# Kernel optimization log

Measured on AMD Instinct MI355X. Metric: run time of the kernel, lower is better.

The kernel has to match this reference:

```python
import jax, jax.numpy as jnp
import numpy as np

N = 8192   # nodes per graph batch
D = 128    # node_feat_dim
E = 131072 # edges per graph batch
B = 64     # graphs per batch


def _linear_init(k, fin, fout):
    s = 1.0 / np.sqrt(fin)
    kw, kb = jax.random.split(k)
    W = jax.random.uniform(kw, (fin, fout), jnp.float32, -s, s)
    b = jax.random.uniform(kb, (fout,), jnp.float32, -s, s)
    return W, b


def setup_inputs() -> dict:
    key = jax.random.key(0)
    ks = jax.random.split(key, 10)
    x1 = jax.random.normal(ks[0], (N, D), jnp.float32)
    x2 = jax.random.normal(ks[1], (N, D), jnp.float32)
    edge_index1 = jax.random.randint(ks[2], (2, E), 0, N)
    edge_index2 = jax.random.randint(ks[3], (2, E), 0, N)
    # block-contiguous graph ids; every graph id present on both sides
    batch = jnp.arange(N, dtype=jnp.int32) // (N // B)
    mW1, mb1 = _linear_init(ks[4], 2 * D, 512)
    mW2, mb2 = _linear_init(ks[5], 512, 256)  # 256 == 2*D (update_net constraint)
    uW1, ub1 = _linear_init(ks[6], 4 * D, 512)
    uW2, ub2 = _linear_init(ks[7], 512, 256)
    uW3, ub3 = _linear_init(ks[8], 256, D)
    return dict(x1=x1, edge_index1=edge_index1, batch1=batch,
                x2=x2, edge_index2=edge_index2, batch2=batch,
                mW1=mW1, mb1=mb1, mW2=mW2, mb2=mb2,
                uW1=uW1, ub1=ub1, uW2=uW2, ub2=ub2, uW3=uW3, ub3=ub3)


def _message_aggr(x, edge_index, mW1, mb1, mW2, mb2):
    tgt, src = edge_index[0], edge_index[1]
    inp = jnp.concatenate([x[src], x[tgt]], axis=-1)          # [E, 2D]
    msg = jax.nn.relu(inp @ mW1 + mb1) @ mW2 + mb2            # [E, 2D]
    return jax.ops.segment_sum(msg, tgt, num_segments=x.shape[0])


def _cross_attention(x1, batch1, x2, batch2):
    scores = x1 @ x2.T                                        # [N1, N2]
    mask = batch1[:, None] == batch2[None, :]
    scores = jnp.where(mask, scores, -jnp.inf)
    att1 = x1 - jax.nn.softmax(scores, axis=1) @ x2
    att2 = x2 - jax.nn.softmax(scores, axis=0).T @ x1
    return att1, att2


def _node_update(x, messages, attentions, uW1, ub1, uW2, ub2, uW3, ub3):
    u = jnp.concatenate([messages, attentions, x], axis=-1)   # [N, 4D]
    h = jax.nn.relu(u @ uW1 + ub1)
    h = jax.nn.relu(h @ uW2 + ub2)
    return x + h @ uW3 + ub3                                  # residual update


def reference(x1, edge_index1, batch1, x2, edge_index2, batch2,
              mW1, mb1, mW2, mb2, uW1, ub1, uW2, ub2, uW3, ub3):
    m1 = _message_aggr(x1, edge_index1, mW1, mb1, mW2, mb2)
    m2 = _message_aggr(x2, edge_index2, mW1, mb1, mW2, mb2)
    a1, a2 = _cross_attention(x1, batch1, x2, batch2)
    new_x1 = _node_update(x1, m1, a1, uW1, ub1, uW2, ub2, uW3, ub3)
    new_x2 = _node_update(x2, m2, a2, uW1, ub1, uW2, ub2, uW3, ub3)
    return new_x1, new_x2
```

## Files before the change

### kernel.cpp

```cpp
#include <hip/hip_runtime.h>
#include <stdint.h>


typedef unsigned short u16;
typedef __bf16 bf16x8 __attribute__((ext_vector_type(8)));
typedef float f32x4 __attribute__((ext_vector_type(4)));

#define NN 8192
#define DD 128
#define EE 131072
#define GS 128
#define NG 64

__device__ __forceinline__ float bf2f(u16 u){
  return __uint_as_float(((uint32_t)u) << 16);
}
__device__ __forceinline__ u16 f2bf(float f){
  uint32_t x = __float_as_uint(f);
  return (u16)((x + 0x7fffu + ((x >> 16) & 1u)) >> 16);
}
__device__ __forceinline__ void gload16(const u16* g, u16* l){
  __builtin_amdgcn_global_load_lds(
      (const __attribute__((address_space(1))) uint32_t*)(uintptr_t)g,
      (__attribute__((address_space(3))) uint32_t*)(uintptr_t)l, 16, 0, 0);
}

template<bool RELU, bool DEGBIAS, bool RES, typename OT>
__device__ __forceinline__ void gemm_body(
    const u16* __restrict__ A, int lda,
    const u16* __restrict__ Wt, const float* __restrict__ bias,
    const int* __restrict__ deg,
    const float* __restrict__ res1, const float* __restrict__ res2,
    OT* __restrict__ out, int ldc, int K, int bx, int by,
    u16* __restrict__ sh, int t)
{
  u16* As0 = sh;         u16* Bs0 = sh + 4096;
  u16* As1 = sh + 8192;  u16* Bs1 = sh + 12288;
  const int brow = by << 7, bcol = bx << 7;
  const int w = t >> 6, lane = t & 63;
  const int rb = (w >> 1) << 6, cb = (w & 1) << 6;
  const int lr = lane & 15, lq = lane >> 4;

  f32x4 acc[4][4];
  #pragma unroll
  for (int i = 0; i < 4; i++)
    #pragma unroll
    for (int j = 0; j < 4; j++) acc[i][j] = (f32x4){0.f, 0.f, 0.f, 0.f};

  const int s0 = t, s1 = t + 256;
  const int sw0 = (((s0 & 3) ^ ((s0 >> 2) & 3)) << 3);
  const int sw1 = (((s1 & 3) ^ ((s1 >> 2) & 3)) << 3);
  const u16* Ag0 = A  + (size_t)(brow + (s0 >> 2)) * lda + sw0;
  const u16* Ag1 = A  + (size_t)(brow + (s1 >> 2)) * lda + sw1;
  const u16* Bg0 = Wt + (size_t)(bcol + (s0 >> 2)) * K   + sw0;
  const u16* Bg1 = Wt + (size_t)(bcol + (s1 >> 2)) * K   + sw1;
  const int d0 = s0 << 3, d1 = s1 << 3;

  auto stage = [&](int kb, u16* Al, u16* Bl){
    gload16(Ag0 + kb, Al + d0);
    gload16(Ag1 + kb, Al + d1);
    gload16(Bg0 + kb, Bl + d0);
    gload16(Bg1 + kb, Bl + d1);
  };
  auto fence = [&](){
    asm volatile("s_waitcnt vmcnt(0)" ::: "memory");
    __builtin_amdgcn_s_barrier();
    __builtin_amdgcn_sched_barrier(0);
  };
  const int swr = ((lq ^ (lr & 3)) << 3);
  auto compute = [&](const u16* Asb, const u16* Bsb){
    bf16x8 af[4], bfr[4];
    #pragma unroll
    for (int mi = 0; mi < 4; mi++)
      af[mi] = *(const bf16x8*)&Asb[(rb + mi * 16 + lr) * 32 + swr];
    #pragma unroll
    for (int ni = 0; ni < 4; ni++)
      bfr[ni] = *(const bf16x8*)&Bsb[(cb + ni * 16 + lr) * 32 + swr];
    #pragma unroll
    for (int mi = 0; mi < 4; mi++)
      #pragma unroll
      for (int ni = 0; ni < 4; ni++)
        acc[mi][ni] = __builtin_amdgcn_mfma_f32_16x16x32_bf16(af[mi], bfr[ni], acc[mi][ni], 0, 0, 0);
  };

  stage(0, As0, Bs0);
  fence();
  for (int kb = 0; kb < K; kb += 64){
    if (kb + 32 < K) stage(kb + 32, As1, Bs1);
    compute(As0, Bs0);
    fence();
    if (kb + 64 < K) stage(kb + 64, As0, Bs0);
    compute(As1, Bs1);
    fence();
  }

  #pragma unroll
  for (int mi = 0; mi < 4; mi++)
    #pragma unroll
    for (int ni = 0; ni < 4; ni++)
      #pragma unroll
      for (int rr = 0; rr < 4; rr++){
        int grow = brow + rb + mi * 16 + lq * 4 + rr;
        int gcol = bcol + cb + ni * 16 + lr;
        float v = acc[mi][ni][rr];
        if (bias) v += DEGBIAS ? (float)deg[grow] * bias[gcol] : bias[gcol];
        if constexpr (RELU) v = fmaxf(v, 0.f);
        if constexpr (RES){
          const float* rp = (grow < NN) ? res1 : res2;
          v += rp[(size_t)(grow & (NN - 1)) * ldc + gcol];
        }
        if constexpr (sizeof(OT) == 2) out[(size_t)grow * ldc + gcol] = (OT)f2bf(v);
        else                           out[(size_t)grow * ldc + gcol] = (OT)v;
      }
}

template<bool RELU, bool RES, typename OT>
__global__ __launch_bounds__(256)
void gemm2_k(const u16* __restrict__ A, int lda,
             const u16* __restrict__ Wt, const float* __restrict__ bias,
             const float* __restrict__ res1, const float* __restrict__ res2,
             OT* __restrict__ out, int ldc, int K)
{
  __shared__ u16 sh[16384];
  gemm_body<RELU,false,RES,OT>(A, lda, Wt, bias, nullptr, res1, res2,
                               out, ldc, K, blockIdx.y, blockIdx.x,
                               sh, threadIdx.x);
}

__global__ __launch_bounds__(256)
void pre_k(const float* __restrict__ mW1, const float* __restrict__ mb1,
           const float* __restrict__ mW2, const float* __restrict__ uW1,
           const float* __restrict__ uW2, const float* __restrict__ uW3,
           const float* __restrict__ x1, const float* __restrict__ x2,
           const int* __restrict__ ei1, const int* __restrict__ ei2,
           u16* __restrict__ WtPQ, float* __restrict__ bPQ,
           u16* __restrict__ Wtm2, u16* __restrict__ Wtu1,
           u16* __restrict__ Wtu2, u16* __restrict__ Wtu3,
           u16* __restrict__ xb, u16* __restrict__ xt,
           u16* __restrict__ U, int* __restrict__ deg)
{
  __shared__ u16 T[8704];
  int b = blockIdx.x, t = threadIdx.x;
  if (b < 2692){
    if (b < 512){
      int idx = b * 256 + t; int c = idx >> 7, k = idx & 127;
      int row = (c < 512) ? k : 128 + k;
      WtPQ[idx] = f2bf(mW1[(size_t)row * 512 + (c & 511)]);
    } else if (b < 1024){
      int idx = (b - 512) * 256 + t; int c = idx >> 9, k = idx & 511;
      Wtm2[idx] = f2bf(mW2[(size_t)k * 256 + c]);
    } else if (b < 2048){
      int idx = (b - 1024) * 256 + t; int c = idx >> 9, k = idx & 511;
      Wtu1[idx] = f2bf(uW1[(size_t)k * 512 + c]);
    } else if (b < 2560){
      int idx = (b - 2048) * 256 + t; int c = idx >> 9, k = idx & 511;
      Wtu2[idx] = f2bf(uW2[(size_t)k * 256 + c]);
    } else if (b < 2688){
      int idx = (b - 2560) * 256 + t; int c = idx >> 8, k = idx & 255;
      Wtu3[idx] = f2bf(uW3[(size_t)k * 128 + c]);
    } else {
      int idx = (b - 2688) * 256 + t;
      bPQ[idx] = (idx < 512) ? 0.f : mb1[idx - 512];
    }
  } else if (b < 4740){
    int a = b - 2692;
    int side = a >> 10, blk = a & 1023;
    const float* x = side ? x2 : x1;
    int i4 = blk * 256 + t;
    float4 v = *(const float4*)&x[(size_t)i4 * 4];
    uint2 pk;
    pk.x = (uint32_t)f2bf(v.x) | ((uint32_t)f2bf(v.y) << 16);
    pk.y = (uint32_t)f2bf(v.z) | ((uint32_t)f2bf(v.w) << 16);
    *(uint2*)&xb[(size_t)side * NN * DD + (size_t)i4 * 4] = pk;
    int n = i4 >> 5, d = (i4 << 2) & 127;
    *(uint2*)&U[((size_t)side * NN + n) * 512 + 384 + d] = pk;
  } else if (b < 4996){
    int a = b - 4740;
    int side = a >> 7, blk = a & 127;
    const float* x = side ? x2 : x1;
    u16* dst = xt + (size_t)side * DD * NN;
    const int n0 = blk * 64;
    #pragma unroll
    for (int i = 0; i < 8; i++){
      int s = i * 256 + t;
      int r = s >> 5, c4 = (s & 31) << 2;
      float4 v = *(const float4*)&x[(size_t)(n0 + r) * DD + c4];
      uint2 pk;
      pk.x = (uint32_t)f2bf(v.x) | ((uint32_t)f2bf(v.y) << 16);
      pk.y = (uint32_t)f2bf(v.z) | ((uint32_t)f2bf(v.w) << 16);
      *(uint2*)&T[r * 136 + c4] = pk;
    }
    __syncthreads();
    #pragma unroll
    for (int i = 0; i < 8; i++){
      int s = i * 256 + t;
      int d = s >> 4, n4 = (s & 15) << 2;
      uint32_t a0 = T[(n4 + 0) * 136 + d];
      uint32_t a1 = T[(n4 + 1) * 136 + d];
      uint32_t a2 = T[(n4 + 2) * 136 + d];
      uint32_t a3 = T[(n4 + 3) * 136 + d];
      uint2 pk; pk.x = a0 | (a1 << 16); pk.y = a2 | (a3 << 16);
      *(uint2*)(dst + (size_t)d * NN + n0 + n4) = pk;
    }
  } else {
    int a = b - 4996;
    int side = a >> 9, blk = a & 511;
    const int* ei = side ? ei2 : ei1;
    int e = blk * 256 + t;
    atomicAdd(&deg[side * NN + ei[e]], 1);
  }
}

__global__ __launch_bounds__(256)
void scan_k(const int* __restrict__ deg,
            int* __restrict__ offs1, int* __restrict__ cur1,
            int* __restrict__ offs2, int* __restrict__ cur2){
  const int* d = deg + blockIdx.x * NN;
  int* offs = blockIdx.x ? offs2 : offs1;
  int* cur  = blockIdx.x ? cur2  : cur1;
  __shared__ int part[256];
  const int t = threadIdx.x;
  const int base = t * 32;
  int loc[32];
  int s = 0;
  #pragma unroll
  for (int i = 0; i < 32; i++){ loc[i] = s; s += d[base + i]; }
  part[t] = s;
  __syncthreads();
  for (int off = 1; off < 256; off <<= 1){
    int v = (t >= off) ? part[t - off] : 0;
    __syncthreads();
    part[t] += v;
    __syncthreads();
  }
  int pre = (t == 0) ? 0 : part[t - 1];
  #pragma unroll
  for (int i = 0; i < 32; i++){
    int o = pre + loc[i];
    offs[base + i] = o;
    cur[base + i]  = o;
  }
  if (t == 255) offs[NN] = part[255];
}

__global__ __launch_bounds__(256)
void mid_k(const u16* __restrict__ xb, const u16* __restrict__ WtPQ,
           const float* __restrict__ bPQ, u16* __restrict__ PQ,
           const int* __restrict__ ei1, const int* __restrict__ ei2,
           int* __restrict__ cur1, int* __restrict__ cur2,
           int* __restrict__ srt1, int* __restrict__ srt2)
{
  __shared__ u16 sh[16384];
  const int b = blockIdx.x, t = threadIdx.x;
  if (b < 1024){
    gemm_body<false,false,false,u16>(xb, 128, WtPQ, bPQ, nullptr, nullptr, nullptr,
                                     PQ, 1024, 128, b >> 7, b & 127, sh, t);
  } else {
    int a = b - 1024;
    int side = a >> 9, blk = a & 511;
    const int* ei = side ? ei2 : ei1;
    int* cur = side ? cur2 : cur1;
    int* srt = side ? srt2 : srt1;
    int e = blk * 256 + t;
    int tgt = ei[e], src = ei[EE + e];
    int p = atomicAdd(&cur[tgt], 1);
    srt[p] = src;
  }
}

__global__ __launch_bounds__(256)
void gather_k(const int* __restrict__ offs1, const int* __restrict__ srt1,
              const int* __restrict__ offs2, const int* __restrict__ srt2,
              const u16* __restrict__ PQ, u16* __restrict__ S)
{
  const int side = blockIdx.y;
  const int* offs = side ? offs2 : offs1;
  const int* srt  = side ? srt2  : srt1;
  const u16* base = PQ + (size_t)side * NN * 1024;
  u16* Sb = S + (size_t)side * NN * 512;

  const int node = (blockIdx.x << 2) + (threadIdx.x >> 6);
  const int lane = threadIdx.x & 63;
  const int beg = offs[node], end = offs[node + 1];

  uint4 qv = *(const uint4*)(base + (size_t)node * 1024 + 512 + (lane << 3));
  float q[8];
  {
    uint32_t qw[4] = {qv.x, qv.y, qv.z, qv.w};
    #pragma unroll
    for (int i = 0; i < 4; i++){
      q[i * 2]     = bf2f((u16)(qw[i] & 0xffffu));
      q[i * 2 + 1] = bf2f((u16)(qw[i] >> 16));
    }
  }
  float acc[8] = {0.f,0.f,0.f,0.f,0.f,0.f,0.f,0.f};

  int e = beg;
  for (; e + 3 < end; e += 4){
    int sA = srt[e], sB = srt[e+1], sC = srt[e+2], sD = srt[e+3];
    uint4 pA = *(const uint4*)(base + (size_t)sA * 1024 + (lane << 3));
    uint4 pB = *(const uint4*)(base + (size_t)sB * 1024 + (lane << 3));
    uint4 pC = *(const uint4*)(base + (size_t)sC * 1024 + (lane << 3));
    uint4 pD = *(const uint4*)(base + (size_t)sD * 1024 + (lane << 3));
    uint32_t aw[4] = {pA.x, pA.y, pA.z, pA.w};
    uint32_t bw[4] = {pB.x, pB.y, pB.z, pB.w};
    uint32_t cw[4] = {pC.x, pC.y, pC.z, pC.w};
    uint32_t dw[4] = {pD.x, pD.y, pD.z, pD.w};
    #pragma unroll
    for (int i = 0; i < 4; i++){
      acc[i*2]   += fmaxf(bf2f((u16)(aw[i] & 0xffffu)) + q[i*2],   0.f)
                  + fmaxf(bf2f((u16)(bw[i] & 0xffffu)) + q[i*2],   0.f)
                  + fmaxf(bf2f((u16)(cw[i] & 0xffffu)) + q[i*2],   0.f)
                  + fmaxf(bf2f((u16)(dw[i] & 0xffffu)) + q[i*2],   0.f);
      acc[i*2+1] += fmaxf(bf2f((u16)(aw[i] >> 16))     + q[i*2+1], 0.f)
                  + fmaxf(bf2f((u16)(bw[i] >> 16))     + q[i*2+1], 0.f)
                  + fmaxf(bf2f((u16)(cw[i] >> 16))     + q[i*2+1], 0.f)
                  + fmaxf(bf2f((u16)(dw[i] >> 16))     + q[i*2+1], 0.f);
    }
  }
  for (; e < end; e++){
    int sA = srt[e];
    uint4 pA = *(const uint4*)(base + (size_t)sA * 1024 + (lane << 3));
    uint32_t aw[4] = {pA.x, pA.y, pA.z, pA.w};
    #pragma unroll
    for (int i = 0; i < 4; i++){
      acc[i*2]   += fmaxf(bf2f((u16)(aw[i] & 0xffffu)) + q[i*2],   0.f);
      acc[i*2+1] += fmaxf(bf2f((u16)(aw[i] >> 16))     + q[i*2+1], 0.f);
    }
  }
  uint4 pk;
  pk.x = (uint32_t)f2bf(acc[0]) | ((uint32_t)f2bf(acc[1]) << 16);
  pk.y = (uint32_t)f2bf(acc[2]) | ((uint32_t)f2bf(acc[3]) << 16);
  pk.z = (uint32_t)f2bf(acc[4]) | ((uint32_t)f2bf(acc[5]) << 16);
  pk.w = (uint32_t)f2bf(acc[6]) | ((uint32_t)f2bf(acc[7]) << 16);
  *(uint4*)(Sb + (size_t)node * 512 + (lane << 3)) = pk;
}

__global__ __launch_bounds__(256)
void msgattn_k(const u16* __restrict__ S, const u16* __restrict__ Wtm2,
               const float* __restrict__ mb2, const int* __restrict__ deg,
               const u16* __restrict__ xb, const u16* __restrict__ xt,
               u16* __restrict__ U)
{
  __shared__ u16 sh[26112];
  const int b = blockIdx.x, t = threadIdx.x;
  if (b < 256){
    gemm_body<false,true,false,u16>(S, 512, Wtm2, mb2, deg, nullptr, nullptr,
                                    U, 512, 512, b >> 7, b & 127, sh, t);
    return;
  }
  const int a = b - 256;
  const int side = a >> 7;
  const int g = a & 63, h = (a >> 6) & 1;
  const u16* Xa = xb + (size_t)side * NN * DD;
  const u16* Xb = xb + (size_t)(1 - side) * NN * DD;
  const u16* Xt = xt + (size_t)(1 - side) * DD * NN;
  u16* Uside = U + (size_t)side * NN * 512;

  u16* XaS = sh;
  u16* XbS = sh + 8704;

  const int w = t >> 6, lane = t & 63;
  const int lr = lane & 15, lq = lane >> 4;

  {
    const u16* sa = Xa + ((size_t)g * GS + h * 64) * DD;
    #pragma unroll
    for (int i = 0; i < 4; i++){
      int s = i * 256 + t; int r = s >> 4, c8 = (s & 15) << 3;
      *(uint4*)&XaS[r * 136 + c8] = *(const uint4*)(sa + (size_t)r * DD + c8);
    }
    const u16* sb = Xb + (size_t)g * GS * DD;
    #pragma unroll
    for (int i = 0; i < 8; i++){
      int s = i * 256 + t; int r = s >> 4, c8 = (s & 15) << 3;
      *(uint4*)&XbS[r * 136 + c8] = *(const uint4*)(sb + (size_t)r * DD + c8);
    }
  }
  __syncthreads();

  f32x4 sc[8];
  #pragma unroll
  for (int ct = 0; ct < 8; ct++) sc[ct] = (f32x4){0.f, 0.f, 0.f, 0.f};
  #pragma unroll
  for (int kb = 0; kb < 4; kb++){
    bf16x8 aa = *(const bf16x8*)&XaS[(w * 16 + lr) * 136 + kb * 32 + (lq << 3)];
    #pragma unroll
    for (int ct = 0; ct < 8; ct++){
      bf16x8 bb = *(const bf16x8*)&XbS[(ct * 16 + lr) * 136 + kb * 32 + (lq << 3)];
      sc[ct] = __builtin_amdgcn_mfma_f32_16x16x32_bf16(aa, bb, sc[ct], 0, 0, 0);
    }
  }
  float inv[4];
  #pragma unroll
  for (int rr = 0; rr < 4; rr++){
    float m = sc[0][rr];
    #pragma unroll
    for (int ct = 1; ct < 8; ct++) m = fmaxf(m, sc[ct][rr]);
    #pragma unroll
    for (int sh_ = 1; sh_ < 16; sh_ <<= 1) m = fmaxf(m, __shfl_xor(m, sh_, 64));
    float s = 0.f;
    #pragma unroll
    for (int ct = 0; ct < 8; ct++){
      float e = __expf(sc[ct][rr] - m);
      sc[ct][rr] = e; s += e;
    }
    #pragma unroll
    for (int sh_ = 1; sh_ < 16; sh_ <<= 1) s += __shfl_xor(s, sh_, 64);
    inv[rr] = 1.f / s;
  }
  #pragma unroll
  for (int ct = 0; ct < 8; ct++)
    #pragma unroll
    for (int rr = 0; rr < 4; rr++)
      XaS[(w * 16 + lq * 4 + rr) * 136 + ct * 16 + lr] = f2bf(sc[ct][rr] * inv[rr]);
  __syncthreads();

  f32x4 o[8];
  #pragma unroll
  for (int ct = 0; ct < 8; ct++) o[ct] = (f32x4){0.f, 0.f, 0.f, 0.f};
  #pragma unroll
  for (int kb = 0; kb < 4; kb++){
    bf16x8 aa = *(const bf16x8*)&XaS[(w * 16 + lr) * 136 + kb * 32 + (lq << 3)];
    #pragma unroll
    for (int ct = 0; ct < 8; ct++){
      bf16x8 bb = *(const bf16x8*)(Xt + (size_t)(ct * 16 + lr) * NN + g * GS + kb * 32 + (lq << 3));
      o[ct] = __builtin_amdgcn_mfma_f32_16x16x32_bf16(aa, bb, o[ct], 0, 0, 0);
    }
  }
  const u16* XaG = Xa + ((size_t)g * GS + h * 64) * DD;
  #pragma unroll
  for (int ct = 0; ct < 8; ct++)
    #pragma unroll
    for (int rr = 0; rr < 4; rr++){
      int row = w * 16 + lq * 4 + rr, col = ct * 16 + lr;
      float xa = bf2f(XaG[(size_t)row * DD + col]);
      Uside[((size_t)g * GS + h * 64 + row) * 512 + 256 + col] = f2bf(xa - o[ct][rr]);
    }
}

extern "C" void kernel_launch(void* const* d_in, const int* in_sizes, int n_in,
                              void* d_out, int out_size, void* d_ws, size_t ws_size,
                              hipStream_t stream)
{
  const float* x1  = (const float*)d_in[0];
  const int*   ei1 = (const int*)  d_in[1];
  const float* x2  = (const float*)d_in[3];
  const int*   ei2 = (const int*)  d_in[4];
  const float* mW1 = (const float*)d_in[6];
  const float* mb1 = (const float*)d_in[7];
  const float* mW2 = (const float*)d_in[8];
  const float* mb2 = (const float*)d_in[9];
  const float* uW1 = (const float*)d_in[10];
  const float* ub1 = (const float*)d_in[11];
  const float* uW2 = (const float*)d_in[12];
  const float* ub2 = (const float*)d_in[13];
  const float* uW3 = (const float*)d_in[14];
  const float* ub3 = (const float*)d_in[15];
  float* out = (float*)d_out;

  char* w = (char*)d_ws;
  auto alloc = [&](size_t b){ char* p = w; w += (b + 255) & ~(size_t)255; return p; };
  u16*  S    = (u16*)alloc((size_t)2 * NN * 512 * 2);
  u16*  PQ   = (u16*)alloc((size_t)2 * NN * 1024 * 2);
  u16*  xb   = (u16*)alloc((size_t)2 * NN * DD * 2);
  u16*  xt   = (u16*)alloc((size_t)2 * DD * NN * 2);
  u16*  U    = (u16*)alloc((size_t)2 * NN * 512 * 2);
  u16*  H1   = (u16*)alloc((size_t)2 * NN * 512 * 2);
  u16*  H2   = (u16*)alloc((size_t)2 * NN * 256 * 2);
  int*  deg  = (int*)alloc((size_t)2 * NN * 4);
  int*  offs1 = (int*)alloc((NN + 1) * 4);
  int*  offs2 = (int*)alloc((NN + 1) * 4);
  int*  cur1  = (int*)alloc(NN * 4);
  int*  cur2  = (int*)alloc(NN * 4);
  int*  srt1  = (int*)alloc((size_t)EE * 4);
  int*  srt2  = (int*)alloc((size_t)EE * 4);
  u16*  WtPQ = (u16*)alloc(1024 * 128 * 2);
  float* bPQ = (float*)alloc(1024 * 4);
  u16*  Wtm2 = (u16*)alloc(256 * 512 * 2);
  u16*  Wtu1 = (u16*)alloc(512 * 512 * 2);
  u16*  Wtu2 = (u16*)alloc(256 * 512 * 2);
  u16*  Wtu3 = (u16*)alloc(128 * 256 * 2);

  hipMemsetAsync(deg, 0, (size_t)2 * NN * 4, stream);

  pre_k<<<4996 + 1024, 256, 0, stream>>>(
      mW1, mb1, mW2, uW1, uW2, uW3, x1, x2, ei1, ei2,
      WtPQ, bPQ, Wtm2, Wtu1, Wtu2, Wtu3, xb, xt, U, deg);

  scan_k<<<2, 256, 0, stream>>>(deg, offs1, cur1, offs2, cur2);

  mid_k<<<2048, 256, 0, stream>>>(xb, WtPQ, bPQ, PQ, ei1, ei2,
                                  cur1, cur2, srt1, srt2);

  gather_k<<<dim3(NN / 4, 2), 256, 0, stream>>>(offs1, srt1, offs2, srt2, PQ, S);

  msgattn_k<<<512, 256, 0, stream>>>(S, Wtm2, mb2, deg, xb, xt, U);

  gemm2_k<true,false,u16><<<dim3(128,4),256,0,stream>>>(
      U, 512, Wtu1, ub1, nullptr, nullptr, H1, 512, 512);
  gemm2_k<true,false,u16><<<dim3(128,2),256,0,stream>>>(
      H1, 512, Wtu2, ub2, nullptr, nullptr, H2, 256, 512);
  gemm2_k<false,true,float><<<dim3(128,1),256,0,stream>>>(
      H2, 256, Wtu3, ub3, x1, x2, out, 128, 256);
}
```

Before: 271.2 us.

## Fuse three node-update GEMMs into one kernel with LDS-resident intermediates

Replaces the three separate update-MLP GEMM launches with a single kernel. Each 512-thread block takes 64 rows and keeps the H1 and H2 activations in shared memory instead of writing them to and reading them back from global memory. The gather loop also gains an 8-edge unrolled path so more independent loads are in flight. The catch is a large LDS footprint (about 138 KB) and only 256 blocks, which lowers occupancy, and each block re-streams the full weight matrices.

```diff
diff --git a/kernel.cpp b/kernel.cpp
--- a/kernel.cpp
+++ b/kernel.cpp
@@ -23,6 +23,11 @@
   __builtin_amdgcn_global_load_lds(
       (const __attribute__((address_space(1))) uint32_t*)(uintptr_t)g,
       (__attribute__((address_space(3))) uint32_t*)(uintptr_t)l, 16, 0, 0);
+}
+__device__ __forceinline__ void gfence(){
+  asm volatile("s_waitcnt vmcnt(0)" ::: "memory");
+  __builtin_amdgcn_s_barrier();
+  __builtin_amdgcn_sched_barrier(0);
 }
 
 template<bool RELU, bool DEGBIAS, bool RES, typename OT>
@@ -62,11 +67,6 @@
     gload16(Bg0 + kb, Bl + d0);
     gload16(Bg1 + kb, Bl + d1);
   };
-  auto fence = [&](){
-    asm volatile("s_waitcnt vmcnt(0)" ::: "memory");
-    __builtin_amdgcn_s_barrier();
-    __builtin_amdgcn_sched_barrier(0);
-  };
   const int swr = ((lq ^ (lr & 3)) << 3);
   auto compute = [&](const u16* Asb, const u16* Bsb){
     bf16x8 af[4], bfr[4];
@@ -84,14 +84,14 @@
   };
 
   stage(0, As0, Bs0);
-  fence();
+  gfence();
   for (int kb = 0; kb < K; kb += 64){
     if (kb + 32 < K) stage(kb + 32, As1, Bs1);
     compute(As0, Bs0);
-    fence();
+    gfence();
     if (kb + 64 < K) stage(kb + 64, As0, Bs0);
     compute(As1, Bs1);
-    fence();
+    gfence();
   }
 
   #pragma unroll
@@ -112,19 +112,6 @@
         if constexpr (sizeof(OT) == 2) out[(size_t)grow * ldc + gcol] = (OT)f2bf(v);
         else                           out[(size_t)grow * ldc + gcol] = (OT)v;
       }
-}
-
-template<bool RELU, bool RES, typename OT>
-__global__ __launch_bounds__(256)
-void gemm2_k(const u16* __restrict__ A, int lda,
-             const u16* __restrict__ Wt, const float* __restrict__ bias,
-             const float* __restrict__ res1, const float* __restrict__ res2,
-             OT* __restrict__ out, int ldc, int K)
-{
-  __shared__ u16 sh[16384];
-  gemm_body<RELU,false,RES,OT>(A, lda, Wt, bias, nullptr, res1, res2,
-                               out, ldc, K, blockIdx.y, blockIdx.x,
-                               sh, threadIdx.x);
 }
 
 __global__ __launch_bounds__(256)
@@ -296,26 +283,40 @@
   float acc[8] = {0.f,0.f,0.f,0.f,0.f,0.f,0.f,0.f};
 
   int e = beg;
+  for (; e + 7 < end; e += 8){
+    int sx[8];
+    #pragma unroll
+    for (int i = 0; i < 8; i++) sx[i] = srt[e + i];
+    uint4 pv[8];
+    #pragma unroll
+    for (int i = 0; i < 8; i++)
+      pv[i] = *(const uint4*)(base + (size_t)sx[i] * 1024 + (lane << 3));
+    #pragma unroll
+    for (int i = 0; i < 8; i++){
+      uint32_t w0[4] = {pv[i].x, pv[i].y, pv[i].z, pv[i].w};
+      #pragma unroll
+      for (int j = 0; j < 4; j++){
+        acc[j*2]   += fmaxf(bf2f((u16)(w0[j] & 0xffffu)) + q[j*2],   0.f);
+        acc[j*2+1] += fmaxf(bf2f((u16)(w0[j] >> 16))     + q[j*2+1], 0.f);
+      }
+    }
+  }
   for (; e + 3 < end; e += 4){
-    int sA = srt[e], sB = srt[e+1], sC = srt[e+2], sD = srt[e+3];
-    uint4 pA = *(const uint4*)(base + (size_t)sA * 1024 + (lane << 3));
-    uint4 pB = *(const uint4*)(base + (size_t)sB * 1024 + (lane << 3));
-    uint4 pC = *(const uint4*)(base + (size_t)sC * 1024 + (lane << 3));
-    uint4 pD = *(const uint4*)(base + (size_t)sD * 1024 + (lane << 3));
-    uint32_t aw[4] = {pA.x, pA.y, pA.z, pA.w};
-    uint32_t bw[4] = {pB.x, pB.y, pB.z, pB.w};
-    uint32_t cw[4] = {pC.x, pC.y, pC.z, pC.w};
-    uint32_t dw[4] = {pD.x, pD.y, pD.z, pD.w};
+    int sx[4];
+    #pragma unroll
+    for (int i = 0; i < 4; i++) sx[i] = srt[e + i];
+    uint4 pv[4];
+    #pragma unroll
+    for (int i = 0; i < 4; i++)
+      pv[i] = *(const uint4*)(base + (size_t)sx[i] * 1024 + (lane << 3));
     #pragma unroll
     for (int i = 0; i < 4; i++){
-      acc[i*2]   += fmaxf(bf2f((u16)(aw[i] & 0xffffu)) + q[i*2],   0.f)
-                  + fmaxf(bf2f((u16)(bw[i] & 0xffffu)) + q[i*2],   0.f)
-                  + fmaxf(bf2f((u16)(cw[i] & 0xffffu)) + q[i*2],   0.f)
-                  + fmaxf(bf2f((u16)(dw[i] & 0xffffu)) + q[i*2],   0.f);
-      acc[i*2+1] += fmaxf(bf2f((u16)(aw[i] >> 16))     + q[i*2+1], 0.f)
-                  + fmaxf(bf2f((u16)(bw[i] >> 16))     + q[i*2+1], 0.f)
-                  + fmaxf(bf2f((u16)(cw[i] >> 16))     + q[i*2+1], 0.f)
-                  + fmaxf(bf2f((u16)(dw[i] >> 16))     + q[i*2+1], 0.f);
+      uint32_t w0[4] = {pv[i].x, pv[i].y, pv[i].z, pv[i].w};
+      #pragma unroll
+      for (int j = 0; j < 4; j++){
+        acc[j*2]   += fmaxf(bf2f((u16)(w0[j] & 0xffffu)) + q[j*2],   0.f);
+        acc[j*2+1] += fmaxf(bf2f((u16)(w0[j] >> 16))     + q[j*2+1], 0.f);
+      }
     }
   }
   for (; e < end; e++){
@@ -437,6 +438,181 @@
       float xa = bf2f(XaG[(size_t)row * DD + col]);
       Uside[((size_t)g * GS + h * 64 + row) * 512 + 256 + col] = f2bf(xa - o[ct][rr]);
     }
+}
+
+__global__ __launch_bounds__(512)
+void upd_k(const u16* __restrict__ U,
+           const u16* __restrict__ Wtu1, const float* __restrict__ ub1,
+           const u16* __restrict__ Wtu2, const float* __restrict__ ub2,
+           const u16* __restrict__ Wtu3, const float* __restrict__ ub3,
+           const float* __restrict__ x1, const float* __restrict__ x2,
+           float* __restrict__ out)
+{
+  __shared__ u16 sh[70656];
+  u16* H1s  = sh;
+  u16* H2s  = sh + 33280;
+  u16* Bst0 = sh + 50176;
+  u16* Bst1 = sh + 58368;
+  u16* Ast0 = sh + 66560;
+  u16* Ast1 = sh + 68608;
+
+  const int t = threadIdx.x;
+  const int w = t >> 6, lane = t & 63;
+  const int wr = w >> 2, wc = w & 3;
+  const int lr = lane & 15, lq = lane >> 4;
+  const int r0 = blockIdx.x << 6;
+
+  const int sA = t;
+  const int rA = sA >> 2;
+  const int swA = (((sA & 3) ^ (rA & 3)) << 3);
+  const int sB0 = t, sB1 = t + 512;
+  const int cB0 = sB0 >> 2, cB1 = sB1 >> 2;
+  const int swB0 = (((sB0 & 3) ^ (cB0 & 3)) << 3);
+  const int swB1 = (((sB1 & 3) ^ (cB1 & 3)) << 3);
+  const int swr = ((lq ^ (lr & 3)) << 3);
+
+  f32x4 acc[2][4];
+  auto zacc = [&](){
+    #pragma unroll
+    for (int i = 0; i < 2; i++)
+      #pragma unroll
+      for (int j = 0; j < 4; j++) acc[i][j] = (f32x4){0.f, 0.f, 0.f, 0.f};
+  };
+
+  for (int hN = 0; hN < 2; hN++){
+    zacc();
+    auto stA = [&](int kb, u16* dst){
+      if (t < 256) gload16(U + (size_t)(r0 + rA) * 512 + kb + swA, dst + sA * 8);
+    };
+    auto stB = [&](int kb, u16* dst){
+      gload16(Wtu1 + (size_t)(hN * 256 + cB0) * 512 + kb + swB0, dst + sB0 * 8);
+      gload16(Wtu1 + (size_t)(hN * 256 + cB1) * 512 + kb + swB1, dst + sB1 * 8);
+    };
+    auto comp = [&](const u16* Asb, const u16* Bsb){
+      bf16x8 af[2], bfv[4];
+      #pragma unroll
+      for (int mi = 0; mi < 2; mi++)
+        af[mi] = *(const bf16x8*)&Asb[(wr * 32 + mi * 16 + lr) * 32 + swr];
+      #pragma unroll
+      for (int ct = 0; ct < 4; ct++)
+        bfv[ct] = *(const bf16x8*)&Bsb[(wc * 64 + ct * 16 + lr) * 32 + swr];
+      #pragma unroll
+      for (int mi = 0; mi < 2; mi++)
+        #pragma unroll
+        for (int ct = 0; ct < 4; ct++)
+          acc[mi][ct] = __builtin_amdgcn_mfma_f32_16x16x32_bf16(af[mi], bfv[ct], acc[mi][ct], 0, 0, 0);
+    };
+    stA(0, Ast0); stB(0, Bst0);
+    gfence();
+    for (int kb = 0; kb < 512; kb += 64){
+      if (kb + 32 < 512){ stA(kb + 32, Ast1); stB(kb + 32, Bst1); }
+      comp(Ast0, Bst0);
+      gfence();
+      if (kb + 64 < 512){ stA(kb + 64, Ast0); stB(kb + 64, Bst0); }
+      comp(Ast1, Bst1);
+      gfence();
+    }
+    #pragma unroll
+    for (int mi = 0; mi < 2; mi++)
+      #pragma unroll
+      for (int ct = 0; ct < 4; ct++)
+        #pragma unroll
+        for (int rr = 0; rr < 4; rr++){
+          int row = wr * 32 + mi * 16 + lq * 4 + rr;
+          int col = wc * 64 + ct * 16 + lr;
+          float v = acc[mi][ct][rr] + ub1[hN * 256 + col];
+          H1s[row * 520 + hN * 256 + col] = f2bf(fmaxf(v, 0.f));
+        }
+  }
+  __syncthreads();
+
+  zacc();
+  {
+    auto stB = [&](int kb, u16* dst){
+      gload16(Wtu2 + (size_t)cB0 * 512 + kb + swB0, dst + sB0 * 8);
+      gload16(Wtu2 + (size_t)cB1 * 512 + kb + swB1, dst + sB1 * 8);
+    };
+    auto comp = [&](int kb, const u16* Bsb){
+      bf16x8 af[2], bfv[4];
+      #pragma unroll
+      for (int mi = 0; mi < 2; mi++)
+        af[mi] = *(const bf16x8*)&H1s[(wr * 32 + mi * 16 + lr) * 520 + kb + (lq << 3)];
+      #pragma unroll
+      for (int ct = 0; ct < 4; ct++)
+        bfv[ct] = *(const bf16x8*)&Bsb[(wc * 64 + ct * 16 + lr) * 32 + swr];
+      #pragma unroll
+      for (int mi = 0; mi < 2; mi++)
+        #pragma unroll
+        for (int ct = 0; ct < 4; ct++)
+          acc[mi][ct] = __builtin_amdgcn_mfma_f32_16x16x32_bf16(af[mi], bfv[ct], acc[mi][ct], 0, 0, 0);
+    };
+    stB(0, Bst0);
+    gfence();
+    for (int kb = 0; kb < 512; kb += 64){
+      if (kb + 32 < 512) stB(kb + 32, Bst1);
+      comp(kb, Bst0);
+      gfence();
+      if (kb + 64 < 512) stB(kb + 64, Bst0);
+      comp(kb + 32, Bst1);
+      gfence();
+    }
+    #pragma unroll
+    for (int mi = 0; mi < 2; mi++)
+      #pragma unroll
+      for (int ct = 0; ct < 4; ct++)
+        #pragma unroll
+        for (int rr = 0; rr < 4; rr++){
+          int row = wr * 32 + mi * 16 + lq * 4 + rr;
+          int col = wc * 64 + ct * 16 + lr;
+          H2s[row * 264 + col] = f2bf(fmaxf(acc[mi][ct][rr] + ub2[col], 0.f));
+        }
+  }
+  __syncthreads();
+
+  zacc();
+  {
+    auto stB = [&](int kb, u16* dst){
+      gload16(Wtu3 + (size_t)cB0 * 256 + kb + swB0, dst + sB0 * 8);
+    };
+    auto comp = [&](int kb, const u16* Bsb){
+      bf16x8 af[2], bfv[2];
+      #pragma unroll
+      for (int mi = 0; mi < 2; mi++)
+        af[mi] = *(const bf16x8*)&H2s[(wr * 32 + mi * 16 + lr) * 264 + kb + (lq << 3)];
+      #pragma unroll
+      for (int ct = 0; ct < 2; ct++)
+        bfv[ct] = *(const bf16x8*)&Bsb[(wc * 32 + ct * 16 + lr) * 32 + swr];
+      #pragma unroll
+      for (int mi = 0; mi < 2; mi++)
+        #pragma unroll
+        for (int ct = 0; ct < 2; ct++)
+          acc[mi][ct] = __builtin_amdgcn_mfma_f32_16x16x32_bf16(af[mi], bfv[ct], acc[mi][ct], 0, 0, 0);
+    };
+    stB(0, Bst0);
+    gfence();
+    for (int kb = 0; kb < 256; kb += 64){
+      if (kb + 32 < 256) stB(kb + 32, Bst1);
+      comp(kb, Bst0);
+      gfence();
+      if (kb + 64 < 256) stB(kb + 64, Bst0);
+      comp(kb + 32, Bst1);
+      gfence();
+    }
+    #pragma unroll
+    for (int mi = 0; mi < 2; mi++)
+      #pragma unroll
+      for (int ct = 0; ct < 2; ct++)
+        #pragma unroll
+        for (int rr = 0; rr < 4; rr++){
+          int row = wr * 32 + mi * 16 + lq * 4 + rr;
+          int col = wc * 32 + ct * 16 + lr;
+          int grow = r0 + row;
+          const float* rp = (grow < NN) ? x1 : x2;
+          float v = acc[mi][ct][rr] + ub3[col]
+                  + rp[(size_t)(grow & (NN - 1)) * 128 + col];
+          out[(size_t)grow * 128 + col] = v;
+        }
+  }
 }
 
 extern "C" void kernel_launch(void* const* d_in, const int* in_sizes, int n_in,
@@ -466,8 +642,6 @@
   u16*  xb   = (u16*)alloc((size_t)2 * NN * DD * 2);
   u16*  xt   = (u16*)alloc((size_t)2 * DD * NN * 2);
   u16*  U    = (u16*)alloc((size_t)2 * NN * 512 * 2);
-  u16*  H1   = (u16*)alloc((size_t)2 * NN * 512 * 2);
-  u16*  H2   = (u16*)alloc((size_t)2 * NN * 256 * 2);
   int*  deg  = (int*)alloc((size_t)2 * NN * 4);
   int*  offs1 = (int*)alloc((NN + 1) * 4);
   int*  offs2 = (int*)alloc((NN + 1) * 4);
@@ -497,10 +671,6 @@
 
   msgattn_k<<<512, 256, 0, stream>>>(S, Wtm2, mb2, deg, xb, xt, U);
 
-  gemm2_k<true,false,u16><<<dim3(128,4),256,0,stream>>>(
-      U, 512, Wtu1, ub1, nullptr, nullptr, H1, 512, 512);
-  gemm2_k<true,false,u16><<<dim3(128,2),256,0,stream>>>(
-      H1, 512, Wtu2, ub2, nullptr, nullptr, H2, 256, 512);
-  gemm2_k<false,true,float><<<dim3(128,1),256,0,stream>>>(
-      H2, 256, Wtu3, ub3, x1, x2, out, 128, 256);
-}
+  upd_k<<<256, 512, 0, stream>>>(U, Wtu1, ub1, Wtu2, ub2, Wtu3, ub3,
+                                 x1, x2, out);
+}
```

Result: faster. 238.8 us (-12.0%).
